# Performance work log

Measured on AMD Instinct MI355X. Metric: run time of the kernel, lower is better.

The kernel has to match this reference:

```python
import jax, jax.numpy as jnp
import numpy as np

N_NODES = 50000
N_EDGES = 800000
NODE_IN = 16
NODE_OUT = 3
H = 128
N_LAYERS = 3


def setup_inputs() -> dict:
    key = jax.random.key(0)
    ks = jax.random.split(key, 16)
    s = 0.05
    inp = {
        "x": jax.random.normal(ks[0], (N_NODES, NODE_IN), dtype=jnp.float32),
        "edge_index": jax.random.randint(ks[1], (2, N_EDGES), 0, N_NODES, dtype=jnp.int64),
        # encoder / decoder
        "enc_w": jax.random.normal(ks[2], (NODE_IN, H), dtype=jnp.float32) * s,
        "enc_b": jnp.zeros((H,), dtype=jnp.float32),
        "dec_w": jax.random.normal(ks[3], (H, NODE_OUT), dtype=jnp.float32) * s,
        "dec_b": jnp.zeros((NODE_OUT,), dtype=jnp.float32),
        # 3 processor layers, edge MLP: Linear(2H,H) -> ReLU -> Linear(H,H)
        "edge_w1": jax.random.normal(ks[4], (N_LAYERS, 2 * H, H), dtype=jnp.float32) * s,
        "edge_b1": jnp.zeros((N_LAYERS, H), dtype=jnp.float32),
        "edge_w2": jax.random.normal(ks[5], (N_LAYERS, H, H), dtype=jnp.float32) * s,
        "edge_b2": jnp.zeros((N_LAYERS, H), dtype=jnp.float32),
        # node MLP: Linear(2H,H) -> ReLU -> Linear(H,H)
        "node_w1": jax.random.normal(ks[6], (N_LAYERS, 2 * H, H), dtype=jnp.float32) * s,
        "node_b1": jnp.zeros((N_LAYERS, H), dtype=jnp.float32),
        "node_w2": jax.random.normal(ks[7], (N_LAYERS, H, H), dtype=jnp.float32) * s,
        "node_b2": jnp.zeros((N_LAYERS, H), dtype=jnp.float32),
    }
    return inp


def reference(x, edge_index, enc_w, enc_b, dec_w, dec_b,
              edge_w1, edge_b1, edge_w2, edge_b2,
              node_w1, node_b1, node_w2, node_b2):
    row = edge_index[0]  # source nodes
    col = edge_index[1]  # destination nodes
    h = x @ enc_w + enc_b  # [N, H]
    for l in range(N_LAYERS):
        # EdgeModel: cat(src, dest) -> MLP
        e_in = jnp.concatenate([h[row], h[col]], axis=1)  # [E, 2H]
        e = jnp.maximum(e_in @ edge_w1[l] + edge_b1[l], 0.0) @ edge_w2[l] + edge_b2[l]  # [E, H]
        # NodeModel: scatter_add messages by col, cat with x -> MLP
        agg = jax.ops.segment_sum(e, col, num_segments=h.shape[0])  # [N, H]
        n_in = jnp.concatenate([h, agg], axis=1)  # [N, 2H]
        h_upd = jnp.maximum(n_in @ node_w1[l] + node_b1[l], 0.0) @ node_w2[l] + node_b2[l]
        h = h + h_upd  # residual
    return h @ dec_w + dec_b  # [N, NODE_OUT]
```

## Files before the change

### kernel.cpp

```cpp
#include <hip/hip_runtime.h>
#include <hip/hip_bf16.h>
#include <stdint.h>

#define N_NODES 50000
#define N_EDGES 800000
#define HID 128
#define NODE_IN 16
#define NODE_OUT 3
#define NODE_TILES 782
#define SCAN_BLOCKS 196
#define EDGE_BLOCKS 3125
#define MFOLD_BLOCKS 192
#define SWZA_BLOCKS 576
#define SWZB_BLOCKS 384
#define EDBLOCKS 6250

typedef __attribute__((ext_vector_type(8))) short short8;
typedef __attribute__((ext_vector_type(4))) float f32x4;
typedef __attribute__((ext_vector_type(4))) unsigned int u32x4;

__device__ __forceinline__ unsigned short f2bf(float f) {
    union { float f; unsigned int u; } v; v.f = f;
    unsigned int u = v.u;
    u += 0x7fff + ((u >> 16) & 1);
    return (unsigned short)(u >> 16);
}
__device__ __forceinline__ float bf2f(unsigned short s) {
    union { unsigned int u; float f; } v; v.u = ((unsigned int)s) << 16;
    return v.f;
}
__device__ __forceinline__ float bfu_lo(unsigned int u) {
    union { unsigned int u; float f; } v; v.u = u << 16; return v.f;
}
__device__ __forceinline__ float bfu_hi(unsigned int u) {
    union { unsigned int u; float f; } v; v.u = u & 0xffff0000u; return v.f;
}
__device__ __forceinline__ unsigned int cvt_pk_bf16(float lo, float hi) {
    unsigned int r;
    asm("v_cvt_pk_bf16_f32 %0, %1, %2" : "=v"(r) : "v"(lo), "v"(hi));
    return r;
}

__global__ __launch_bounds__(256) void k1_fused(
    const int* __restrict__ colp, int* __restrict__ cnt, int* __restrict__ rank,
    const float* __restrict__ edge_w2, const float* __restrict__ node_w1,
    const float* __restrict__ edge_b2,
    float* __restrict__ Mtmp, float* __restrict__ Vtmp,
    const float* __restrict__ x, const float* __restrict__ enc_w,
    const float* __restrict__ enc_b, unsigned short* __restrict__ h,
    const float* __restrict__ edge_w1, const float* __restrict__ node_w2,
    unsigned short* __restrict__ swz) {
    __shared__ float wts[NODE_IN * HID];
    __shared__ float bts[HID];
    __shared__ float xs[64][NODE_IN];
    int b = blockIdx.x, t = threadIdx.x;
    if (b < EDGE_BLOCKS) {
        int e = b * 256 + t;
        rank[e] = atomicAdd(&cnt[colp[e]], 1);
    } else if (b < EDGE_BLOCKS + MFOLD_BLOCKS) {
        int d = (b - EDGE_BLOCKS) * 256 + t;
        int L = d / 16384, rem = d & 16383;
        int k = rem >> 7, n = rem & 127;
        const float* w2  = edge_w2 + (size_t)L * 16384;
        const float* w1b = node_w1 + (size_t)L * 32768 + 16384;
        float acc = 0.f;
        #pragma unroll 4
        for (int j = 0; j < 128; j++) acc += w2[k * 128 + j] * w1b[j * 128 + n];
        Mtmp[d] = acc;
        if (k == 0) {
            const float* b2 = edge_b2 + (size_t)L * 128;
            float vv = 0.f;
            #pragma unroll 4
            for (int j = 0; j < 128; j++) vv += b2[j] * w1b[j * 128 + n];
            Vtmp[L * 128 + n] = vv;
        }
    } else if (b < EDGE_BLOCKS + MFOLD_BLOCKS + NODE_TILES) {
        int b2 = b - EDGE_BLOCKS - MFOLD_BLOCKS;
        int n0 = b2 * 64;
        for (int i = t; i < NODE_IN * HID; i += 256) wts[i] = enc_w[i];
        if (t < HID) bts[t] = enc_b[t];
        for (int i = t; i < 64 * NODE_IN; i += 256) {
            int nl = i >> 4, ii = i & 15;
            int n = n0 + nl;
            xs[nl][ii] = (n < N_NODES) ? x[n * NODE_IN + ii] : 0.f;
        }
        __syncthreads();
        for (int o = t; o < 64 * HID; o += 256) {
            int nl = o >> 7, cc = o & 127;
            float acc = bts[cc];
            #pragma unroll
            for (int i = 0; i < NODE_IN; i++) acc += xs[nl][i] * wts[i * HID + cc];
            int n = n0 + nl;
            if (n < N_NODES) h[n * HID + cc] = f2bf(acc);
        }
    } else {
        int d = (b - EDGE_BLOCKS - MFOLD_BLOCKS - NODE_TILES) * 256 + t;
        int L = d / 49152, rem2 = d - L * 49152;
        unsigned short* base = swz + L * 98304;
        if (rem2 < 32768) {
            const float* w1 = edge_w1 + (size_t)L * 32768;
            int j = rem2 & 7, ll = (rem2 >> 3) & 63, tt = rem2 >> 9;
            int nt = tt & 15, kt = tt >> 4;
            int k = kt * 32 + ((ll >> 4) << 3) + j;
            int cc = nt * 16 + (ll & 15);
            float v = (cc < 128) ? w1[k * 128 + cc] : w1[(128 + k) * 128 + (cc - 128)];
            base[rem2] = f2bf(v);
        } else {
            int d2 = rem2 - 32768;
            const float* src = node_w2 + (size_t)L * 16384;
            int j = d2 & 7, ll = (d2 >> 3) & 63, tt = d2 >> 9;
            int nt = tt & 7, kt = tt >> 3;
            int k = kt * 32 + ((ll >> 4) << 3) + j, n = (nt << 4) + (ll & 15);
            base[81920 + d2] = f2bf(src[k * 128 + n]);
        }
    }
}

__global__ __launch_bounds__(256) void k2a_scan1_swizzle(
    const int* __restrict__ cnt, int* __restrict__ ex, int* __restrict__ bsums,
    const float* __restrict__ node_w1, const float* __restrict__ Mtmp,
    unsigned short* __restrict__ swz) {
    __shared__ int s[256];
    int b = blockIdx.x, t = threadIdx.x;
    if (b < SCAN_BLOCKS) {
        int i = b * 256 + t;
        int v = (i < N_NODES) ? cnt[i] : 0;
        s[t] = v;
        __syncthreads();
        for (int off = 1; off < 256; off <<= 1) {
            int u = (t >= off) ? s[t - off] : 0;
            __syncthreads();
            s[t] += u;
            __syncthreads();
        }
        if (i < N_NODES) ex[i] = s[t] - v;
        if (t == 255) bsums[b] = s[255];
    } else {
        int d = (b - SCAN_BLOCKS) * 256 + t;
        int L = d / 32768, d2 = d - L * 32768;
        unsigned short* base = swz + L * 98304;
        int j = d2 & 7, ll = (d2 >> 3) & 63, tt = d2 >> 9;
        int nt = tt & 7, kt = tt >> 3;
        int k = kt * 32 + ((ll >> 4) << 3) + j, n = (nt << 4) + (ll & 15);
        float v = (k < 128) ? node_w1[(size_t)L * 32768 + k * 128 + n]
                            : Mtmp[(size_t)L * 16384 + (k - 128) * 128 + n];
        base[49152 + d2] = f2bf(v);
    }
}

__global__ __launch_bounds__(256) void k3_scatter_sd(
    const int* __restrict__ rowp, const int* __restrict__ colp,
    const int* __restrict__ ex, const int* __restrict__ bsums,
    const int* __restrict__ rank, int* __restrict__ rsrt, int* __restrict__ ex2,
    const unsigned short* __restrict__ h, const unsigned short* __restrict__ w1c,
    const float* __restrict__ eb1,
    unsigned short* __restrict__ S, unsigned short* __restrict__ D) {
    __shared__ int sc[256];
    __shared__ int ls[SCAN_BLOCKS];
    __shared__ unsigned short hs[64][136];
    int b = blockIdx.x, t = threadIdx.x;
    if (b < EDGE_BLOCKS) {
        int v = (t < SCAN_BLOCKS) ? bsums[t] : 0;
        sc[t] = v;
        __syncthreads();
        for (int off = 1; off < 256; off <<= 1) {
            int u = (t >= off) ? sc[t - off] : 0;
            __syncthreads();
            sc[t] += u;
            __syncthreads();
        }
        if (t < SCAN_BLOCKS) ls[t] = sc[t] - v;
        __syncthreads();

        if (b < SCAN_BLOCKS) {
            int i = b * 256 + t;
            if (i < N_NODES) ex2[i] = ex[i] + ls[b];
        }
        int e = b * 256 + t;
        int c = colp[e];
        int pos = ex[c] + ls[c >> 8] + rank[e];
        rsrt[pos] = rowp[e];
    } else {
        int b2 = b - EDGE_BLOCKS;
        int wave = t >> 6, l = t & 63, q = l >> 4, l16 = l & 15;
        int nt0s = wave * 4;
        int n0 = b2 * 64;
        for (int i = t; i < 64 * 16; i += 256) {
            int nl = i >> 4, li = i & 15;
            int n = n0 + nl;
            short8 v = (short8){0, 0, 0, 0, 0, 0, 0, 0};
            if (n < N_NODES) v = *(const short8*)(h + (size_t)n * HID + li * 8);
            *(short8*)&hs[nl][li * 8] = v;
        }
        short8 wr[4][4];
        #pragma unroll
        for (int kt = 0; kt < 4; kt++)
            #pragma unroll
            for (int i = 0; i < 4; i++)
                wr[kt][i] = *(const short8*)(w1c + ((kt * 16 + nt0s + i) * 64 + l) * 8);
        __syncthreads();

        f32x4 acc[4][4];
        #pragma unroll
        for (int g = 0; g < 4; g++)
            #pragma unroll
            for (int i = 0; i < 4; i++) acc[g][i] = (f32x4){0.f, 0.f, 0.f, 0.f};
        #pragma unroll
        for (int kt = 0; kt < 4; kt++) {
            #pragma unroll
            for (int g = 0; g < 4; g++) {
                short8 a = *(const short8*)&hs[g * 16 + l16][kt * 32 + q * 8];
                #pragma unroll
                for (int i = 0; i < 4; i++)
                    acc[g][i] = __builtin_amdgcn_mfma_f32_16x16x32_bf16(a, wr[kt][i], acc[g][i], 0, 0, 0);
            }
        }
        #pragma unroll
        for (int i = 0; i < 4; i++) {
            int cc = (nt0s + i) * 16 + l16;
            float badd = 0.f;
            if (cc >= 128) badd = eb1[cc - 128];
            #pragma unroll
            for (int g = 0; g < 4; g++)
                #pragma unroll
                for (int r = 0; r < 4; r++) {
                    int n = n0 + g * 16 + q * 4 + r;
                    if (n < N_NODES) {
                        unsigned short v = f2bf(acc[g][i][r] + badd);
                        if (cc < 128) S[n * HID + cc] = v;
                        else          D[n * HID + (cc - 128)] = v;
                    }
                }
        }
    }
}

__global__ __launch_bounds__(256, 8) void edge_kernel(
    const unsigned short* __restrict__ S, const unsigned short* __restrict__ D,
    const int* __restrict__ rsrt, const int* __restrict__ ex2,
    unsigned short* __restrict__ aggB)
{
    int t = threadIdx.x;
    int g32 = t >> 5, ch = t & 31;

    const int q = EDBLOCKS / 8, r = EDBLOCKS % 8;
    int xcd = blockIdx.x & 7, slot = blockIdx.x >> 3;
    int cntx = q + (xcd < r);
    if (slot >= cntx) return;
    int myb = xcd * q + (xcd < r ? xcd : r) + slot;

    int d = myb * 8 + g32;
    int e0 = ex2[d];
    int e1 = (d < N_NODES - 1) ? ex2[d + 1] : N_EDGES;

    int2 dv = *(const int2*)(D + (size_t)d * HID + ch * 4);
    float dr0 = bfu_lo((unsigned int)dv.x), dr1 = bfu_hi((unsigned int)dv.x);
    float dr2 = bfu_lo((unsigned int)dv.y), dr3 = bfu_hi((unsigned int)dv.y);
    float a0 = 0.f, a1 = 0.f, a2 = 0.f, a3 = 0.f;

    auto Srow = [&](int rn) -> int2 {
        return *(const int2*)(S + (size_t)rn * HID + ch * 4);
    };
    auto accum = [&](int2 sv) {
        float v0 = bfu_lo((unsigned int)sv.x) + dr0;
        float v1 = bfu_hi((unsigned int)sv.x) + dr1;
        float v2 = bfu_lo((unsigned int)sv.y) + dr2;
        float v3 = bfu_hi((unsigned int)sv.y) + dr3;
        a0 += v0 > 0.f ? v0 : 0.f;
        a1 += v1 > 0.f ? v1 : 0.f;
        a2 += v2 > 0.f ? v2 : 0.f;
        a3 += v3 > 0.f ? v3 : 0.f;
    };
    const int2 z = make_int2(0, 0);

    int2 c0 = z, c1 = z, c2 = z, c3 = z;
    int rb0 = 0, rb1 = 0, rb2 = 0, rb3 = 0;
    {
        int ra0 = (e0     < e1) ? rsrt[e0]     : 0;
        int ra1 = (e0 + 1 < e1) ? rsrt[e0 + 1] : 0;
        int ra2 = (e0 + 2 < e1) ? rsrt[e0 + 2] : 0;
        int ra3 = (e0 + 3 < e1) ? rsrt[e0 + 3] : 0;
        rb0 = (e0 + 4 < e1) ? rsrt[e0 + 4] : 0;
        rb1 = (e0 + 5 < e1) ? rsrt[e0 + 5] : 0;
        rb2 = (e0 + 6 < e1) ? rsrt[e0 + 6] : 0;
        rb3 = (e0 + 7 < e1) ? rsrt[e0 + 7] : 0;
        if (e0     < e1) c0 = Srow(ra0);
        if (e0 + 1 < e1) c1 = Srow(ra1);
        if (e0 + 2 < e1) c2 = Srow(ra2);
        if (e0 + 3 < e1) c3 = Srow(ra3);
    }

    int e = e0;
    while (e + 12 <= e1) {
        int m0 = rsrt[e + 8], m1 = rsrt[e + 9];
        int2 f0 = Srow(rb0), f1 = Srow(rb1);
        accum(c0); accum(c1);
        int m2 = rsrt[e + 10], m3 = rsrt[e + 11];
        int2 f2 = Srow(rb2), f3 = Srow(rb3);
        accum(c2); accum(c3);
        c0 = f0; c1 = f1; c2 = f2; c3 = f3;
        rb0 = m0; rb1 = m1; rb2 = m2; rb3 = m3;
        e += 4;
    }
    int rem = e1 - e;
    if (rem > 0) accum(c0);
    if (rem > 1) accum(c1);
    if (rem > 2) accum(c2);
    if (rem > 3) accum(c3);
    if (rem > 4) accum(Srow(rb0));
    if (rem > 5) accum(Srow(rb1));
    if (rem > 6) accum(Srow(rb2));
    if (rem > 7) accum(Srow(rb3));
    for (int j = 8; j < rem; j++) accum(Srow(rsrt[e + j]));

    int2 o = make_int2((int)cvt_pk_bf16(a0, a1), (int)cvt_pk_bf16(a2, a3));
    *(int2*)(aggB + (size_t)d * HID + ch * 4) = o;
}

template<int LAST>
__global__ __launch_bounds__(256, 4) void node_kernel(
    unsigned short* __restrict__ h, const unsigned short* __restrict__ aggB,
    const int* __restrict__ cnt,
    const unsigned short* __restrict__ w1m_s, const float* __restrict__ b1,
    const float* __restrict__ vfold,
    const unsigned short* __restrict__ w2s, const float* __restrict__ b2,
    const unsigned short* __restrict__ w1c_next, const float* __restrict__ eb1n,
    unsigned short* __restrict__ S, unsigned short* __restrict__ D,
    const float* __restrict__ dec_w, const float* __restrict__ dec_b, float* __restrict__ out)
{
    __shared__ unsigned short in_h[64][136];
    __shared__ unsigned short in_a[64][136];
    __shared__ int cnt_s[64];
    __shared__ float dw[HID * NODE_OUT];
    __shared__ float db[NODE_OUT];
    int t = threadIdx.x, wave = t >> 6, l = t & 63, q = l >> 4, l16 = l & 15;
    int nt0 = wave * 2, nt0s = wave * 4;
    int n0 = blockIdx.x * 64;

    if (LAST) {
        for (int i = t; i < HID * NODE_OUT; i += 256) dw[i] = dec_w[i];
        if (t < NODE_OUT) db[t] = dec_b[t];
    }

    #pragma unroll
    for (int it = 0; it < 8; it++) {
        int g = it * 256 + t;
        int nl = g >> 5, sub = g & 31, half = sub >> 4, li = sub & 15;
        int n = n0 + nl;
        short8 v = (short8){0, 0, 0, 0, 0, 0, 0, 0};
        if (n < N_NODES) {
            if (half == 0) v = *(const short8*)(h + (size_t)n * HID + li * 8);
            else           v = *(const short8*)(aggB + (size_t)n * HID + li * 8);
        }
        if (half == 0) *(short8*)&in_h[nl][li * 8] = v;
        else           *(short8*)&in_a[nl][li * 8] = v;
    }
    if (t < 64) cnt_s[t] = (n0 + t < N_NODES) ? cnt[n0 + t] : 0;
    __syncthreads();

    float b1r0 = b1[nt0 * 16 + l16], b1r1 = b1[(nt0 + 1) * 16 + l16];
    float vr0 = vfold[nt0 * 16 + l16], vr1 = vfold[(nt0 + 1) * 16 + l16];
    float b2r0 = b2[nt0 * 16 + l16], b2r1 = b2[(nt0 + 1) * 16 + l16];

    f32x4 acc[4][2];
    #pragma unroll
    for (int g = 0; g < 4; g++)
        #pragma unroll
        for (int j = 0; j < 2; j++) acc[g][j] = (f32x4){0.f, 0.f, 0.f, 0.f};
    #pragma unroll
    for (int kt = 0; kt < 8; kt++) {
        short8 b0 = *(const short8*)(w1m_s + ((kt * 8 + nt0)     * 64 + l) * 8);
        short8 b1v = *(const short8*)(w1m_s + ((kt * 8 + nt0 + 1) * 64 + l) * 8);
        #pragma unroll
        for (int g = 0; g < 4; g++) {
            short8 a = (kt < 4) ? *(const short8*)&in_h[g * 16 + l16][kt * 32 + q * 8]
                                : *(const short8*)&in_a[g * 16 + l16][(kt - 4) * 32 + q * 8];
            acc[g][0] = __builtin_amdgcn_mfma_f32_16x16x32_bf16(a, b0, acc[g][0], 0, 0, 0);
            acc[g][1] = __builtin_amdgcn_mfma_f32_16x16x32_bf16(a, b1v, acc[g][1], 0, 0, 0);
        }
    }
    __syncthreads();

    #pragma unroll
    for (int j = 0; j < 2; j++) {
        float bv = j ? b1r1 : b1r0;
        float vv = j ? vr1 : vr0;
        #pragma unroll
        for (int g = 0; g < 4; g++)
            #pragma unroll
            for (int r = 0; r < 4; r++) {
                int m2 = g * 16 + q * 4 + r;
                float v = acc[g][j][r] + bv + (float)cnt_s[m2] * vv;
                v = v > 0.f ? v : 0.f;
                in_a[m2][(nt0 + j) * 16 + l16] = f2bf(v);
            }
    }
    __syncthreads();

    f32x4 acc2[4][2];
    #pragma unroll
    for (int g = 0; g < 4; g++)
        #pragma unroll
        for (int j = 0; j < 2; j++) acc2[g][j] = (f32x4){0.f, 0.f, 0.f, 0.f};
    #pragma unroll
    for (int kt = 0; kt < 4; kt++) {
        short8 b0 = *(const short8*)(w2s + ((kt * 8 + nt0)     * 64 + l) * 8);
        short8 b1v = *(const short8*)(w2s + ((kt * 8 + nt0 + 1) * 64 + l) * 8);
        #pragma unroll
        for (int g = 0; g < 4; g++) {
            short8 a = *(const short8*)&in_a[g * 16 + l16][kt * 32 + q * 8];
            acc2[g][0] = __builtin_amdgcn_mfma_f32_16x16x32_bf16(a, b0, acc2[g][0], 0, 0, 0);
            acc2[g][1] = __builtin_amdgcn_mfma_f32_16x16x32_bf16(a, b1v, acc2[g][1], 0, 0, 0);
        }
    }
    #pragma unroll
    for (int j = 0; j < 2; j++) {
        float bv = j ? b2r1 : b2r0;
        #pragma unroll
        for (int g = 0; g < 4; g++)
            #pragma unroll
            for (int r = 0; r < 4; r++) {
                float v = acc2[g][j][r] + bv;
                int m2 = g * 16 + q * 4 + r;
                int n = n0 + m2;
                if (n < N_NODES) {
                    int c = (nt0 + j) * 16 + l16;
                    unsigned short nh = f2bf(bf2f(in_h[m2][c]) + v);
                    if (!LAST) h[n * HID + c] = nh;
                    in_h[m2][c] = nh;
                }
            }
    }
    __syncthreads();

    if (!LAST) {
        #pragma unroll
        for (int p = 0; p < 2; p++) {
            short8 wr[4][2];
            #pragma unroll
            for (int kt = 0; kt < 4; kt++) {
                wr[kt][0] = *(const short8*)(w1c_next + ((kt * 16 + nt0s + p * 2)     * 64 + l) * 8);
                wr[kt][1] = *(const short8*)(w1c_next + ((kt * 16 + nt0s + p * 2 + 1) * 64 + l) * 8);
            }
            f32x4 accs[4][2];
            #pragma unroll
            for (int g = 0; g < 4; g++)
                #pragma unroll
                for (int i = 0; i < 2; i++) accs[g][i] = (f32x4){0.f, 0.f, 0.f, 0.f};
            #pragma unroll
            for (int kt = 0; kt < 4; kt++) {
                #pragma unroll
                for (int g = 0; g < 4; g++) {
                    short8 a = *(const short8*)&in_h[g * 16 + l16][kt * 32 + q * 8];
                    accs[g][0] = __builtin_amdgcn_mfma_f32_16x16x32_bf16(a, wr[kt][0], accs[g][0], 0, 0, 0);
                    accs[g][1] = __builtin_amdgcn_mfma_f32_16x16x32_bf16(a, wr[kt][1], accs[g][1], 0, 0, 0);
                }
            }
            #pragma unroll
            for (int i = 0; i < 2; i++) {
                int c = (nt0s + p * 2 + i) * 16 + l16;
                float badd = 0.f;
                if (c >= 128) badd = eb1n[c - 128];
                #pragma unroll
                for (int g = 0; g < 4; g++)
                    #pragma unroll
                    for (int r = 0; r < 4; r++) {
                        int n = n0 + g * 16 + q * 4 + r;
                        if (n < N_NODES) {
                            unsigned short v = f2bf(accs[g][i][r] + badd);
                            if (c < 128) S[n * HID + c] = v;
                            else         D[n * HID + (c - 128)] = v;
                        }
                    }
            }
        }
    } else {
        if (t < 64 * NODE_OUT) {
            int nl = t / 3, o = t - 3 * nl;
            int n = n0 + nl;
            if (n < N_NODES) {
                float a = db[o];
                #pragma unroll 4
                for (int k = 0; k < HID; k++) a += bf2f(in_h[nl][k]) * dw[k * 3 + o];
                out[n * 3 + o] = a;
            }
        }
    }
}

extern "C" void kernel_launch(void* const* d_in, const int* in_sizes, int n_in,
                              void* d_out, int out_size, void* d_ws, size_t ws_size,
                              hipStream_t stream) {
    const float* x       = (const float*)d_in[0];
    const int*   ei      = (const int*)d_in[1];
    const float* enc_w   = (const float*)d_in[2];
    const float* enc_b   = (const float*)d_in[3];
    const float* dec_w   = (const float*)d_in[4];
    const float* dec_b   = (const float*)d_in[5];
    const float* edge_w1 = (const float*)d_in[6];
    const float* edge_b1 = (const float*)d_in[7];
    const float* edge_w2 = (const float*)d_in[8];
    const float* edge_b2 = (const float*)d_in[9];
    const float* node_w1 = (const float*)d_in[10];
    const float* node_b1 = (const float*)d_in[11];
    const float* node_w2 = (const float*)d_in[12];
    const float* node_b2 = (const float*)d_in[13];

    char* ws = (char*)d_ws;
    unsigned short* h    = (unsigned short*)ws;
    unsigned short* aggB = (unsigned short*)(ws + 12800000);
    unsigned short* swz  = (unsigned short*)(ws + 25600000);
    int* cnt             = (int*)(ws + 26189824);
    int* ex              = (int*)(ws + 26389824);
    int* bsums           = (int*)(ws + 26589824);
    int* rsrt            = (int*)(ws + 26590848);
    unsigned short* Sbuf = (unsigned short*)(ws + 29790848);
    unsigned short* Dbuf = (unsigned short*)(ws + 42590848);
    float* Mtmp          = (float*)(ws + 55390848);
    float* Vtmp          = (float*)(ws + 55587456);
    int* ex2             = (int*)(ws + 55588992);
    int* rank            = (int*)(ws + 55788992);

    const int* rowp = ei;
    const int* colp = ei + N_EDGES;

    hipMemsetAsync(cnt, 0, (size_t)N_NODES * 4, stream);

    k1_fused<<<EDGE_BLOCKS + MFOLD_BLOCKS + NODE_TILES + SWZA_BLOCKS, 256, 0, stream>>>(
        colp, cnt, rank, edge_w2, node_w1, edge_b2, Mtmp, Vtmp,
        x, enc_w, enc_b, h, edge_w1, node_w2, swz);
    k2a_scan1_swizzle<<<SCAN_BLOCKS + SWZB_BLOCKS, 256, 0, stream>>>(
        cnt, ex, bsums, node_w1, Mtmp, swz);
    k3_scatter_sd<<<EDGE_BLOCKS + NODE_TILES, 256, 0, stream>>>(
        rowp, colp, ex, bsums, rank, rsrt, ex2,
        h, swz , edge_b1 , Sbuf, Dbuf);

    for (int L = 0; L < 3; L++) {
        unsigned short* base = swz + (size_t)L * 98304;
        unsigned short* next = swz + (size_t)(L + 1) * 98304;
        edge_kernel<<<6256, 256, 0, stream>>>(Sbuf, Dbuf, rsrt, ex2, aggB);
        if (L < 2) {
            node_kernel<0><<<NODE_TILES, 256, 0, stream>>>(
                h, aggB, cnt,
                base + 49152, node_b1 + (size_t)L * HID, Vtmp + (size_t)L * HID,
                base + 81920, node_b2 + (size_t)L * HID,
                next, edge_b1 + (size_t)(L + 1) * HID, Sbuf, Dbuf, dec_w, dec_b, (float*)d_out);
        } else {
            node_kernel<1><<<NODE_TILES, 256, 0, stream>>>(
                h, aggB, cnt,
                base + 49152, node_b1 + (size_t)L * HID, Vtmp + (size_t)L * HID,
                base + 81920, node_b2 + (size_t)L * HID,
                base , edge_b1 , Sbuf, Dbuf, dec_w, dec_b, (float*)d_out);
        }
    }
}
```

Before: 351.8 us.

## Shard degree counters per XCD and fuse first-layer S/D projection into encoder

The per-destination atomic counter is split into 8 copies indexed by block mod 8, which spreads atomic contention across XCDs. A per-shard prefix step in the scan kernel produces shard bases and a total count, and the scatter adds the shard base to each edge's rank. The first layer's S/D projection moves into the encoder tiles of k1, which build the bf16 weight fragments directly from fp32 edge_w1 and reuse the freshly computed h from LDS. That removes the separate S/D blocks from k3 and one round-trip of h, at the cost of extra memset and counter traffic and heavier register use in k1.

```diff
diff --git a/kernel.cpp b/kernel.cpp
--- a/kernel.cpp
+++ b/kernel.cpp
@@ -42,21 +42,25 @@
 }
 
 __global__ __launch_bounds__(256) void k1_fused(
-    const int* __restrict__ colp, int* __restrict__ cnt, int* __restrict__ rank,
+    const int* __restrict__ colp, int* __restrict__ cnt8, int* __restrict__ rank,
     const float* __restrict__ edge_w2, const float* __restrict__ node_w1,
     const float* __restrict__ edge_b2,
     float* __restrict__ Mtmp, float* __restrict__ Vtmp,
     const float* __restrict__ x, const float* __restrict__ enc_w,
     const float* __restrict__ enc_b, unsigned short* __restrict__ h,
     const float* __restrict__ edge_w1, const float* __restrict__ node_w2,
-    unsigned short* __restrict__ swz) {
+    unsigned short* __restrict__ swz,
+    const float* __restrict__ eb1,
+    unsigned short* __restrict__ S, unsigned short* __restrict__ D) {
     __shared__ float wts[NODE_IN * HID];
     __shared__ float bts[HID];
     __shared__ float xs[64][NODE_IN];
+    __shared__ unsigned short hs[64][136];
     int b = blockIdx.x, t = threadIdx.x;
     if (b < EDGE_BLOCKS) {
         int e = b * 256 + t;
-        rank[e] = atomicAdd(&cnt[colp[e]], 1);
+        int c = colp[e];
+        rank[e] = atomicAdd(&cnt8[(size_t)(b & 7) * N_NODES + c], 1);
     } else if (b < EDGE_BLOCKS + MFOLD_BLOCKS) {
         int d = (b - EDGE_BLOCKS) * 256 + t;
         int L = d / 16384, rem = d & 16383;
@@ -76,7 +80,10 @@
         }
     } else if (b < EDGE_BLOCKS + MFOLD_BLOCKS + NODE_TILES) {
         int b2 = b - EDGE_BLOCKS - MFOLD_BLOCKS;
+        int wave = t >> 6, l = t & 63, q = l >> 4, l16 = l & 15;
+        int nt0s = wave * 4;
         int n0 = b2 * 64;
+
         for (int i = t; i < NODE_IN * HID; i += 256) wts[i] = enc_w[i];
         if (t < HID) bts[t] = enc_b[t];
         for (int i = t; i < 64 * NODE_IN; i += 256) {
@@ -84,14 +91,65 @@
             int n = n0 + nl;
             xs[nl][ii] = (n < N_NODES) ? x[n * NODE_IN + ii] : 0.f;
         }
+        short8 wr[4][4];
+        #pragma unroll
+        for (int kt = 0; kt < 4; kt++)
+            #pragma unroll
+            for (int i = 0; i < 4; i++) {
+                int ccol = (nt0s + i) * 16 + l16;
+                #pragma unroll
+                for (int j = 0; j < 8; j++) {
+                    int k = kt * 32 + ((l >> 4) << 3) + j;
+                    float v = (ccol < 128) ? edge_w1[k * 128 + ccol]
+                                           : edge_w1[(128 + k) * 128 + (ccol - 128)];
+                    ((unsigned short*)&wr[kt][i])[j] = f2bf(v);
+                }
+            }
         __syncthreads();
+
         for (int o = t; o < 64 * HID; o += 256) {
             int nl = o >> 7, cc = o & 127;
             float acc = bts[cc];
             #pragma unroll
             for (int i = 0; i < NODE_IN; i++) acc += xs[nl][i] * wts[i * HID + cc];
+            unsigned short hb = f2bf(acc);
+            hs[nl][cc] = hb;
             int n = n0 + nl;
-            if (n < N_NODES) h[n * HID + cc] = f2bf(acc);
+            if (n < N_NODES) h[n * HID + cc] = hb;
+        }
+        __syncthreads();
+
+        f32x4 acc[4][4];
+        #pragma unroll
+        for (int g = 0; g < 4; g++)
+            #pragma unroll
+            for (int i = 0; i < 4; i++) acc[g][i] = (f32x4){0.f, 0.f, 0.f, 0.f};
+        #pragma unroll
+        for (int kt = 0; kt < 4; kt++) {
+            #pragma unroll
+            for (int g = 0; g < 4; g++) {
+                short8 a = *(const short8*)&hs[g * 16 + l16][kt * 32 + q * 8];
+                #pragma unroll
+                for (int i = 0; i < 4; i++)
+                    acc[g][i] = __builtin_amdgcn_mfma_f32_16x16x32_bf16(a, wr[kt][i], acc[g][i], 0, 0, 0);
+            }
+        }
+        #pragma unroll
+        for (int i = 0; i < 4; i++) {
+            int cc = (nt0s + i) * 16 + l16;
+            float badd = 0.f;
+            if (cc >= 128) badd = eb1[cc - 128];
+            #pragma unroll
+            for (int g = 0; g < 4; g++)
+                #pragma unroll
+                for (int r = 0; r < 4; r++) {
+                    int n = n0 + g * 16 + q * 4 + r;
+                    if (n < N_NODES) {
+                        unsigned short v = f2bf(acc[g][i][r] + badd);
+                        if (cc < 128) S[n * HID + cc] = v;
+                        else          D[n * HID + (cc - 128)] = v;
+                    }
+                }
         }
     } else {
         int d = (b - EDGE_BLOCKS - MFOLD_BLOCKS - NODE_TILES) * 256 + t;
@@ -117,15 +175,25 @@
 }
 
 __global__ __launch_bounds__(256) void k2a_scan1_swizzle(
-    const int* __restrict__ cnt, int* __restrict__ ex, int* __restrict__ bsums,
+    const int* __restrict__ cnt8, int* __restrict__ base8, int* __restrict__ cntt,
+    int* __restrict__ ex, int* __restrict__ bsums,
     const float* __restrict__ node_w1, const float* __restrict__ Mtmp,
     unsigned short* __restrict__ swz) {
     __shared__ int s[256];
     int b = blockIdx.x, t = threadIdx.x;
     if (b < SCAN_BLOCKS) {
         int i = b * 256 + t;
-        int v = (i < N_NODES) ? cnt[i] : 0;
-        s[t] = v;
+        int tot = 0;
+        if (i < N_NODES) {
+            #pragma unroll
+            for (int s2 = 0; s2 < 8; s2++) {
+                int v = cnt8[(size_t)s2 * N_NODES + i];
+                base8[(size_t)s2 * N_NODES + i] = tot;
+                tot += v;
+            }
+            cntt[i] = tot;
+        }
+        s[t] = tot;
         __syncthreads();
         for (int off = 1; off < 256; off <<= 1) {
             int u = (t >= off) ? s[t - off] : 0;
@@ -133,7 +201,7 @@
             s[t] += u;
             __syncthreads();
         }
-        if (i < N_NODES) ex[i] = s[t] - v;
+        if (i < N_NODES) ex[i] = s[t] - tot;
         if (t == 255) bsums[b] = s[255];
     } else {
         int d = (b - SCAN_BLOCKS) * 256 + t;
@@ -148,91 +216,35 @@
     }
 }
 
-__global__ __launch_bounds__(256) void k3_scatter_sd(
+__global__ __launch_bounds__(256) void k3_scatter(
     const int* __restrict__ rowp, const int* __restrict__ colp,
     const int* __restrict__ ex, const int* __restrict__ bsums,
-    const int* __restrict__ rank, int* __restrict__ rsrt, int* __restrict__ ex2,
-    const unsigned short* __restrict__ h, const unsigned short* __restrict__ w1c,
-    const float* __restrict__ eb1,
-    unsigned short* __restrict__ S, unsigned short* __restrict__ D) {
+    const int* __restrict__ rank, const int* __restrict__ base8,
+    int* __restrict__ rsrt, int* __restrict__ ex2) {
     __shared__ int sc[256];
     __shared__ int ls[SCAN_BLOCKS];
-    __shared__ unsigned short hs[64][136];
     int b = blockIdx.x, t = threadIdx.x;
-    if (b < EDGE_BLOCKS) {
-        int v = (t < SCAN_BLOCKS) ? bsums[t] : 0;
-        sc[t] = v;
+    int v = (t < SCAN_BLOCKS) ? bsums[t] : 0;
+    sc[t] = v;
+    __syncthreads();
+    for (int off = 1; off < 256; off <<= 1) {
+        int u = (t >= off) ? sc[t - off] : 0;
         __syncthreads();
-        for (int off = 1; off < 256; off <<= 1) {
-            int u = (t >= off) ? sc[t - off] : 0;
-            __syncthreads();
-            sc[t] += u;
-            __syncthreads();
-        }
-        if (t < SCAN_BLOCKS) ls[t] = sc[t] - v;
+        sc[t] += u;
         __syncthreads();
-
-        if (b < SCAN_BLOCKS) {
-            int i = b * 256 + t;
-            if (i < N_NODES) ex2[i] = ex[i] + ls[b];
-        }
-        int e = b * 256 + t;
-        int c = colp[e];
-        int pos = ex[c] + ls[c >> 8] + rank[e];
-        rsrt[pos] = rowp[e];
-    } else {
-        int b2 = b - EDGE_BLOCKS;
-        int wave = t >> 6, l = t & 63, q = l >> 4, l16 = l & 15;
-        int nt0s = wave * 4;
-        int n0 = b2 * 64;
-        for (int i = t; i < 64 * 16; i += 256) {
-            int nl = i >> 4, li = i & 15;
-            int n = n0 + nl;
-            short8 v = (short8){0, 0, 0, 0, 0, 0, 0, 0};
-            if (n < N_NODES) v = *(const short8*)(h + (size_t)n * HID + li * 8);
-            *(short8*)&hs[nl][li * 8] = v;
-        }
-        short8 wr[4][4];
-        #pragma unroll
-        for (int kt = 0; kt < 4; kt++)
-            #pragma unroll
-            for (int i = 0; i < 4; i++)
-                wr[kt][i] = *(const short8*)(w1c + ((kt * 16 + nt0s + i) * 64 + l) * 8);
-        __syncthreads();
-
-        f32x4 acc[4][4];
-        #pragma unroll
-        for (int g = 0; g < 4; g++)
-            #pragma unroll
-            for (int i = 0; i < 4; i++) acc[g][i] = (f32x4){0.f, 0.f, 0.f, 0.f};
-        #pragma unroll
-        for (int kt = 0; kt < 4; kt++) {
-            #pragma unroll
-            for (int g = 0; g < 4; g++) {
-                short8 a = *(const short8*)&hs[g * 16 + l16][kt * 32 + q * 8];
-                #pragma unroll
-                for (int i = 0; i < 4; i++)
-                    acc[g][i] = __builtin_amdgcn_mfma_f32_16x16x32_bf16(a, wr[kt][i], acc[g][i], 0, 0, 0);
-            }
-        }
-        #pragma unroll
-        for (int i = 0; i < 4; i++) {
-            int cc = (nt0s + i) * 16 + l16;
-            float badd = 0.f;
-            if (cc >= 128) badd = eb1[cc - 128];
-            #pragma unroll
-            for (int g = 0; g < 4; g++)
-                #pragma unroll
-                for (int r = 0; r < 4; r++) {
-                    int n = n0 + g * 16 + q * 4 + r;
-                    if (n < N_NODES) {
-                        unsigned short v = f2bf(acc[g][i][r] + badd);
-                        if (cc < 128) S[n * HID + cc] = v;
-                        else          D[n * HID + (cc - 128)] = v;
-                    }
-                }
-        }
-    }
+    }
+    if (t < SCAN_BLOCKS) ls[t] = sc[t] - v;
+    __syncthreads();
+
+    if (b < SCAN_BLOCKS) {
+        int i = b * 256 + t;
+        if (i < N_NODES) ex2[i] = ex[i] + ls[b];
+    }
+    int e = b * 256 + t;
+    int c = colp[e];
+    int sh = b & 7;
+    int pos = ex[c] + ls[c >> 8] + base8[(size_t)sh * N_NODES + c] + rank[e];
+    rsrt[pos] = rowp[e];
 }
 
 __global__ __launch_bounds__(256, 8) void edge_kernel(
@@ -510,30 +522,32 @@
     unsigned short* h    = (unsigned short*)ws;
     unsigned short* aggB = (unsigned short*)(ws + 12800000);
     unsigned short* swz  = (unsigned short*)(ws + 25600000);
-    int* cnt             = (int*)(ws + 26189824);
-    int* ex              = (int*)(ws + 26389824);
-    int* bsums           = (int*)(ws + 26589824);
-    int* rsrt            = (int*)(ws + 26590848);
-    unsigned short* Sbuf = (unsigned short*)(ws + 29790848);
-    unsigned short* Dbuf = (unsigned short*)(ws + 42590848);
-    float* Mtmp          = (float*)(ws + 55390848);
-    float* Vtmp          = (float*)(ws + 55587456);
-    int* ex2             = (int*)(ws + 55588992);
-    int* rank            = (int*)(ws + 55788992);
+    int* cnt8            = (int*)(ws + 26189824);
+    int* base8           = (int*)(ws + 27789824);
+    int* cntt            = (int*)(ws + 29389824);
+    int* ex              = (int*)(ws + 29589824);
+    int* bsums           = (int*)(ws + 29789824);
+    int* rsrt            = (int*)(ws + 29790848);
+    unsigned short* Sbuf = (unsigned short*)(ws + 32990848);
+    unsigned short* Dbuf = (unsigned short*)(ws + 45790848);
+    float* Mtmp          = (float*)(ws + 58590848);
+    float* Vtmp          = (float*)(ws + 58787456);
+    int* ex2             = (int*)(ws + 58788992);
+    int* rank            = (int*)(ws + 58988992);
 
     const int* rowp = ei;
     const int* colp = ei + N_EDGES;
 
-    hipMemsetAsync(cnt, 0, (size_t)N_NODES * 4, stream);
+    hipMemsetAsync(cnt8, 0, (size_t)8 * N_NODES * 4, stream);
 
     k1_fused<<<EDGE_BLOCKS + MFOLD_BLOCKS + NODE_TILES + SWZA_BLOCKS, 256, 0, stream>>>(
-        colp, cnt, rank, edge_w2, node_w1, edge_b2, Mtmp, Vtmp,
-        x, enc_w, enc_b, h, edge_w1, node_w2, swz);
+        colp, cnt8, rank, edge_w2, node_w1, edge_b2, Mtmp, Vtmp,
+        x, enc_w, enc_b, h, edge_w1, node_w2, swz,
+        edge_b1 , Sbuf, Dbuf);
     k2a_scan1_swizzle<<<SCAN_BLOCKS + SWZB_BLOCKS, 256, 0, stream>>>(
-        cnt, ex, bsums, node_w1, Mtmp, swz);
-    k3_scatter_sd<<<EDGE_BLOCKS + NODE_TILES, 256, 0, stream>>>(
-        rowp, colp, ex, bsums, rank, rsrt, ex2,
-        h, swz , edge_b1 , Sbuf, Dbuf);
+        cnt8, base8, cntt, ex, bsums, node_w1, Mtmp, swz);
+    k3_scatter<<<EDGE_BLOCKS, 256, 0, stream>>>(
+        rowp, colp, ex, bsums, rank, base8, rsrt, ex2);
 
     for (int L = 0; L < 3; L++) {
         unsigned short* base = swz + (size_t)L * 98304;
@@ -541,13 +555,13 @@
         edge_kernel<<<6256, 256, 0, stream>>>(Sbuf, Dbuf, rsrt, ex2, aggB);
         if (L < 2) {
             node_kernel<0><<<NODE_TILES, 256, 0, stream>>>(
-                h, aggB, cnt,
+                h, aggB, cntt,
                 base + 49152, node_b1 + (size_t)L * HID, Vtmp + (size_t)L * HID,
                 base + 81920, node_b2 + (size_t)L * HID,
                 next, edge_b1 + (size_t)(L + 1) * HID, Sbuf, Dbuf, dec_w, dec_b, (float*)d_out);
         } else {
             node_kernel<1><<<NODE_TILES, 256, 0, stream>>>(
-                h, aggB, cnt,
+                h, aggB, cntt,
                 base + 49152, node_b1 + (size_t)L * HID, Vtmp + (size_t)L * HID,
                 base + 81920, node_b2 + (size_t)L * HID,
                 base , edge_b1 , Sbuf, Dbuf, dec_w, dec_b, (float*)d_out);
```

Result: slower. 361.5 us (+2.8%).
